# Optimization experiments

Measured on AMD Instinct MI355X. Metric: run time of the kernel, lower is better.

Reference implementation:

```python
import jax, jax.numpy as jnp
import numpy as np

N_NODES = 50000


def _relgraphconv(x, W, Wloop, b, src, dst, etypes, n_nodes):
    # DGL RelGraphConv (regularizer=None, self_loop=True, norm=None):
    # out[i] = sum over incoming edges (j->i, rel r) of W_r @ x[j]  +  W_loop @ x[i]  +  b
    # low-mem form: transform all nodes per relation, then gather per edge.
    h_rel = jnp.einsum('ni,rio->rno', x, W)          # [R, N, out]
    msg = h_rel[etypes, src]                          # [E, out]
    agg = jax.ops.segment_sum(msg, dst, num_segments=n_nodes)  # [N, out]
    return agg + x @ Wloop + b


def setup_inputs() -> dict:
    key = jax.random.key(0)
    ks = jax.random.split(key, 12)
    N, E, n_state = N_NODES, 800000, 128
    inp = {
        'x': jax.random.normal(ks[0], (N, n_state), dtype=jnp.float32),
        'src': jax.random.randint(ks[1], (E,), 0, N, dtype=jnp.int32),
        'dst': jax.random.randint(ks[2], (E,), 0, N, dtype=jnp.int32),
        'etypes': jax.random.randint(ks[3], (E,), 0, 2, dtype=jnp.int32),
        'cell_size': jax.random.randint(ks[4], (N,), 0, 8, dtype=jnp.int32),
        'max_size': jax.random.randint(ks[5], (N,), 0, 8, dtype=jnp.int32),
        'W1': jax.random.normal(ks[6], (2, n_state, 64), dtype=jnp.float32) * 0.05,
        'loop1': jax.random.normal(ks[7], (n_state, 64), dtype=jnp.float32) * 0.05,
        'b1': jnp.zeros((64,), dtype=jnp.float32),
        'W2': jax.random.normal(ks[8], (2, 64, 64), dtype=jnp.float32) * 0.05,
        'loop2': jax.random.normal(ks[9], (64, 64), dtype=jnp.float32) * 0.05,
        'b2': jnp.zeros((64,), dtype=jnp.float32),
        'W3': jax.random.normal(ks[10], (2, 64, 2), dtype=jnp.float32) * 0.05,
        'loop3': jax.random.normal(ks[11], (64, 2), dtype=jnp.float32) * 0.05,
        'b3': jnp.zeros((2,), dtype=jnp.float32),
    }
    return inp


def reference(x, src, dst, etypes, cell_size, max_size,
              W1, loop1, b1, W2, loop2, b2, W3, loop3, b3):
    N = x.shape[0]
    h = jax.nn.relu(_relgraphconv(x, W1, loop1, b1, src, dst, etypes, N))
    h = jax.nn.relu(_relgraphconv(h, W2, loop2, b2, src, dst, etypes, N))
    h = _relgraphconv(h, W3, loop3, b3, src, dst, etypes, N)   # [N, 2]
    # action mask: col 0 = cannot upsize, col 1 = cannot downsize
    upper = cell_size >= (max_size - 1)
    lower = cell_size == 0
    mask = jnp.stack([upper, lower], axis=1)                   # [N, 2] bool
    return jnp.where(mask, h.min() - 1.0, h)
```

## Files before the change

### kernel.cpp

```cpp
#include <hip/hip_runtime.h>


#define STRIDE 64

typedef unsigned short ushortT;

__device__ inline ushortT f2bf(float f) {
    union { float f; unsigned u; } v; v.f = f;
    unsigned r = v.u + 0x7FFFu + ((v.u >> 16) & 1u);
    return (ushortT)(r >> 16);
}
__device__ inline float bf2f(ushortT h) {
    union { unsigned u; float f; } v; v.u = ((unsigned)h) << 16;
    return v.f;
}

__device__ inline void atomicMinF(float* addr, float v) {
    if (v >= 0.f) atomicMin((int*)addr, __float_as_int(v));
    else          atomicMax((unsigned int*)addr, __float_as_uint(v));
}

__global__ __launch_bounds__(256) void mega1_kernel(
    const float* __restrict__ x, const float* __restrict__ W1,
    const float* __restrict__ loop1, const float* __restrict__ b1,
    ushortT* __restrict__ hrelb, ushortT* __restrict__ H1b,
    const int* __restrict__ src, const int* __restrict__ dst,
    const int* __restrict__ et, int* __restrict__ cnt, int* __restrict__ eidx,
    int N, int E) {
    if (blockIdx.x & 1) {
        int g = (int)(blockIdx.x >> 1);
        int e0 = g * 1024 + (int)threadIdx.x;
        int e1 = e0 + 256, e2 = e0 + 512, e3 = e0 + 768;
        bool a0 = e0 < E, a1 = e1 < E, a2 = e2 < E, a3 = e3 < E;
        int d0 = a0 ? dst[e0] : 0, d1 = a1 ? dst[e1] : 0;
        int d2 = a2 ? dst[e2] : 0, d3 = a3 ? dst[e3] : 0;
        int v0 = a0 ? (et[e0] * N + src[e0]) : 0;
        int v1 = a1 ? (et[e1] * N + src[e1]) : 0;
        int v2 = a2 ? (et[e2] * N + src[e2]) : 0;
        int v3 = a3 ? (et[e3] * N + src[e3]) : 0;
        int p0 = 0, p1 = 0, p2 = 0, p3 = 0;
        if (a0) p0 = atomicAdd(&cnt[d0], 1);
        if (a1) p1 = atomicAdd(&cnt[d1], 1);
        if (a2) p2 = atomicAdd(&cnt[d2], 1);
        if (a3) p3 = atomicAdd(&cnt[d3], 1);
        if (a0 && p0 < STRIDE) eidx[(size_t)d0 * STRIDE + p0] = v0;
        if (a1 && p1 < STRIDE) eidx[(size_t)d1 * STRIDE + p1] = v1;
        if (a2 && p2 < STRIDE) eidx[(size_t)d2 * STRIDE + p2] = v2;
        if (a3 && p3 < STRIDE) eidx[(size_t)d3 * STRIDE + p3] = v3;
        return;
    }
    __shared__ float xs[64][64];
    __shared__ ushortT wsb[3][64][68];
    const int tile = (int)(blockIdx.x >> 1);
    const int nbase = tile * 64;
    const int t = (int)threadIdx.x;
    const int tx = t & 15, ty = t >> 4;

    float acc[3][4][4];
#pragma unroll
    for (int m = 0; m < 3; ++m)
#pragma unroll
        for (int j = 0; j < 4; ++j)
#pragma unroll
            for (int i = 0; i < 4; ++i) acc[m][j][i] = 0.f;

    for (int kt = 0; kt < 2; ++kt) {
#pragma unroll
        for (int j = 0; j < 4; ++j) {
            int i = t + j * 256;
            int node = i >> 4;
            int kk4 = (i & 15) * 4;
            int n = nbase + node;
            float4 g = make_float4(0.f, 0.f, 0.f, 0.f);
            if (n < N) g = *(const float4*)&x[(size_t)n * 128 + kt * 64 + kk4];
            int pc = (node + kk4) & 63;
            xs[kk4 + 0][pc] = g.x;
            xs[kk4 + 1][pc] = g.y;
            xs[kk4 + 2][pc] = g.z;
            xs[kk4 + 3][pc] = g.w;
        }
#pragma unroll
        for (int j = 0; j < 12; ++j) {
            int i = t + j * 256;
            int mat = i >> 10;
            int rc = i & 1023;
            int kk = rc >> 4;
            int c4 = (rc & 15) * 4;
            const float* Wm = (mat < 2) ? (W1 + ((size_t)mat * 128 + kt * 64 + kk) * 64 + c4)
                                        : (loop1 + ((size_t)kt * 64 + kk) * 64 + c4);
            float4 g = *(const float4*)Wm;
            ushort4 o;
            o.x = f2bf(g.x); o.y = f2bf(g.y); o.z = f2bf(g.z); o.w = f2bf(g.w);
            *(ushort4*)&wsb[mat][kk][c4] = o;
        }
        __syncthreads();

#pragma unroll 4
        for (int kk = 0; kk < 64; ++kk) {
            int kb = kk & ~3;
            float4 a = *(const float4*)&xs[kk][(ty * 4 + kb) & 63];
#pragma unroll
            for (int m = 0; m < 3; ++m) {
                ushort4 wu = *(const ushort4*)&wsb[m][kk][tx * 4];
                float w0 = bf2f(wu.x), w1 = bf2f(wu.y), w2 = bf2f(wu.z), w3 = bf2f(wu.w);
                acc[m][0][0] += a.x * w0; acc[m][0][1] += a.x * w1; acc[m][0][2] += a.x * w2; acc[m][0][3] += a.x * w3;
                acc[m][1][0] += a.y * w0; acc[m][1][1] += a.y * w1; acc[m][1][2] += a.y * w2; acc[m][1][3] += a.y * w3;
                acc[m][2][0] += a.z * w0; acc[m][2][1] += a.z * w1; acc[m][2][2] += a.z * w2; acc[m][2][3] += a.z * w3;
                acc[m][3][0] += a.w * w0; acc[m][3][1] += a.w * w1; acc[m][3][2] += a.w * w2; acc[m][3][3] += a.w * w3;
            }
        }
        __syncthreads();
    }

    float b0 = b1[tx * 4 + 0], bb1 = b1[tx * 4 + 1], b2v = b1[tx * 4 + 2], b3v = b1[tx * 4 + 3];
#pragma unroll
    for (int j = 0; j < 4; ++j) {
        int n = nbase + ty * 4 + j;
        if (n < N) {
#pragma unroll
            for (int m = 0; m < 2; ++m) {
                ushort4 o;
                o.x = f2bf(acc[m][j][0]); o.y = f2bf(acc[m][j][1]);
                o.z = f2bf(acc[m][j][2]); o.w = f2bf(acc[m][j][3]);
                *(ushort4*)&hrelb[((size_t)m * N + n) * 64 + tx * 4] = o;
            }
            ushort4 h;
            h.x = f2bf(acc[2][j][0] + b0);  h.y = f2bf(acc[2][j][1] + bb1);
            h.z = f2bf(acc[2][j][2] + b2v); h.w = f2bf(acc[2][j][3] + b3v);
            *(ushort4*)&H1b[(size_t)n * 64 + tx * 4] = h;
        }
    }
}

__global__ void agg1_kernel(const ushortT* __restrict__ hrelb, const int* __restrict__ eidx,
                            const int* __restrict__ cnt, ushortT* __restrict__ H1b, int N) {
    int node = (int)blockIdx.x * 4 + ((int)threadIdx.x >> 6);
    if (node >= N) return;
    int lane = (int)threadIdx.x & 63;
    int deg = min(cnt[node], STRIDE);
    int my = (lane < deg) ? eidx[(size_t)node * STRIDE + lane] : 0;
    float acc = bf2f(H1b[(size_t)node * 64 + lane]);
    int j = 0;
    for (; j + 3 < deg; j += 4) {
        int i0 = __shfl(my, j, 64), i1 = __shfl(my, j + 1, 64);
        int i2 = __shfl(my, j + 2, 64), i3 = __shfl(my, j + 3, 64);
        float v0 = bf2f(hrelb[(size_t)i0 * 64 + lane]);
        float v1 = bf2f(hrelb[(size_t)i1 * 64 + lane]);
        float v2 = bf2f(hrelb[(size_t)i2 * 64 + lane]);
        float v3 = bf2f(hrelb[(size_t)i3 * 64 + lane]);
        acc += (v0 + v1) + (v2 + v3);
    }
    for (; j < deg; ++j)
        acc += bf2f(hrelb[(size_t)__shfl(my, j, 64) * 64 + lane]);
    H1b[(size_t)node * 64 + lane] = f2bf(fmaxf(acc, 0.f));
}

__global__ __launch_bounds__(256) void gemm2_kernel(
    const ushortT* __restrict__ H1b,
    const float* __restrict__ W2, const float* __restrict__ loop2,
    const float* __restrict__ b2,
    ushortT* __restrict__ hrel2b, float* __restrict__ H2, int N) {
    __shared__ float xs[64][65];
    __shared__ ushortT wsb[3][64][68];
    const int t = (int)threadIdx.x;
    const int nbase = (int)blockIdx.x * 64;

#pragma unroll
    for (int j = 0; j < 12; ++j) {
        int i = t + j * 256;
        int mat = i >> 10;
        int rc = i & 1023;
        int kk = rc >> 4;
        int c4 = (rc & 15) * 4;
        const float* Wm = (mat < 2) ? (W2 + ((size_t)mat * 64 + kk) * 64 + c4)
                                    : (loop2 + (size_t)kk * 64 + c4);
        float4 g = *(const float4*)Wm;
        ushort4 o;
        o.x = f2bf(g.x); o.y = f2bf(g.y); o.z = f2bf(g.z); o.w = f2bf(g.w);
        *(ushort4*)&wsb[mat][kk][c4] = o;
    }
#pragma unroll
    for (int j = 0; j < 4; ++j) {
        int i = t + j * 256;
        int node = i >> 4;
        int k4 = (i & 15) * 4;
        int n = nbase + node;
        ushort4 g = make_ushort4(0, 0, 0, 0);
        if (n < N) g = *(const ushort4*)&H1b[(size_t)n * 64 + k4];
        xs[node][k4 + 0] = bf2f(g.x);
        xs[node][k4 + 1] = bf2f(g.y);
        xs[node][k4 + 2] = bf2f(g.z);
        xs[node][k4 + 3] = bf2f(g.w);
    }
    __syncthreads();

    const int tx = t & 15, ty = t >> 4;
    float acc2[3][4][4];
#pragma unroll
    for (int m = 0; m < 3; ++m)
#pragma unroll
        for (int j = 0; j < 4; ++j)
#pragma unroll
            for (int i = 0; i < 4; ++i) acc2[m][j][i] = 0.f;

#pragma unroll 4
    for (int kk = 0; kk < 64; ++kk) {
        float a0 = xs[ty * 4 + 0][kk];
        float a1 = xs[ty * 4 + 1][kk];
        float a2 = xs[ty * 4 + 2][kk];
        float a3 = xs[ty * 4 + 3][kk];
#pragma unroll
        for (int m = 0; m < 3; ++m) {
            ushort4 wu = *(const ushort4*)&wsb[m][kk][tx * 4];
            float w0 = bf2f(wu.x), w1 = bf2f(wu.y), w2 = bf2f(wu.z), w3 = bf2f(wu.w);
            acc2[m][0][0] += a0 * w0; acc2[m][0][1] += a0 * w1; acc2[m][0][2] += a0 * w2; acc2[m][0][3] += a0 * w3;
            acc2[m][1][0] += a1 * w0; acc2[m][1][1] += a1 * w1; acc2[m][1][2] += a1 * w2; acc2[m][1][3] += a1 * w3;
            acc2[m][2][0] += a2 * w0; acc2[m][2][1] += a2 * w1; acc2[m][2][2] += a2 * w2; acc2[m][2][3] += a2 * w3;
            acc2[m][3][0] += a3 * w0; acc2[m][3][1] += a3 * w1; acc2[m][3][2] += a3 * w2; acc2[m][3][3] += a3 * w3;
        }
    }

    float b0 = b2[tx * 4 + 0], bb1 = b2[tx * 4 + 1], b2v = b2[tx * 4 + 2], b3v = b2[tx * 4 + 3];
#pragma unroll
    for (int j = 0; j < 4; ++j) {
        int n = nbase + ty * 4 + j;
        if (n < N) {
#pragma unroll
            for (int m = 0; m < 2; ++m) {
                ushort4 o;
                o.x = f2bf(acc2[m][j][0]); o.y = f2bf(acc2[m][j][1]);
                o.z = f2bf(acc2[m][j][2]); o.w = f2bf(acc2[m][j][3]);
                *(ushort4*)&hrel2b[((size_t)m * N + n) * 64 + tx * 4] = o;
            }
            float4 h = make_float4(acc2[2][j][0] + b0, acc2[2][j][1] + bb1,
                                   acc2[2][j][2] + b2v, acc2[2][j][3] + b3v);
            *(float4*)&H2[(size_t)n * 64 + tx * 4] = h;
        }
    }
}

__global__ void k3_kernel(const ushortT* __restrict__ hrel2b, const float* __restrict__ H2,
                          const int* __restrict__ eidx, const int* __restrict__ cnt,
                          const float* __restrict__ W3, const float* __restrict__ loop3,
                          const float* __restrict__ b3,
                          float* __restrict__ hrel3, float* __restrict__ H3, int N) {
    int node = (int)blockIdx.x * 4 + ((int)threadIdx.x >> 6);
    if (node >= N) return;
    int lane = (int)threadIdx.x & 63;
    int deg = min(cnt[node], STRIDE);
    int my = (lane < deg) ? eidx[(size_t)node * STRIDE + lane] : 0;
    float acc = H2[(size_t)node * 64 + lane];
    int j = 0;
    for (; j + 3 < deg; j += 4) {
        int i0 = __shfl(my, j, 64), i1 = __shfl(my, j + 1, 64);
        int i2 = __shfl(my, j + 2, 64), i3 = __shfl(my, j + 3, 64);
        float v0 = bf2f(hrel2b[(size_t)i0 * 64 + lane]);
        float v1 = bf2f(hrel2b[(size_t)i1 * 64 + lane]);
        float v2 = bf2f(hrel2b[(size_t)i2 * 64 + lane]);
        float v3 = bf2f(hrel2b[(size_t)i3 * 64 + lane]);
        acc += (v0 + v1) + (v2 + v3);
    }
    for (; j < deg; ++j)
        acc += bf2f(hrel2b[(size_t)__shfl(my, j, 64) * 64 + lane]);
    float xk = fmaxf(acc, 0.f);
    float p[6];
    p[0] = xk * W3[lane * 2 + 0];
    p[1] = xk * W3[lane * 2 + 1];
    p[2] = xk * W3[(64 + lane) * 2 + 0];
    p[3] = xk * W3[(64 + lane) * 2 + 1];
    p[4] = xk * loop3[lane * 2 + 0];
    p[5] = xk * loop3[lane * 2 + 1];
#pragma unroll
    for (int m = 32; m >= 1; m >>= 1) {
#pragma unroll
        for (int q = 0; q < 6; ++q) p[q] += __shfl_xor(p[q], m, 64);
    }
    if (lane == 0) {
        hrel3[(size_t)node * 2 + 0] = p[0];
        hrel3[(size_t)node * 2 + 1] = p[1];
        hrel3[((size_t)N + node) * 2 + 0] = p[2];
        hrel3[((size_t)N + node) * 2 + 1] = p[3];
        H3[(size_t)node * 2 + 0] = p[4] + b3[0];
        H3[(size_t)node * 2 + 1] = p[5] + b3[1];
    }
}

__global__ void agg3min_kernel(const float* __restrict__ hrel3, const int* __restrict__ eidx,
                               const int* __restrict__ cnt, float* __restrict__ H3,
                               float* __restrict__ minval, int N) {
    int n = (int)blockIdx.x * 256 + (int)threadIdx.x;
    float v = 3.4e38f;
    if (n < N) {
        float a0 = H3[n * 2 + 0], a1 = H3[n * 2 + 1];
        int deg = min(cnt[n], STRIDE);
        const int* row = &eidx[(size_t)n * STRIDE];
        int j = 0;
        for (; j + 3 < deg; j += 4) {
            int i0 = row[j], i1 = row[j + 1], i2 = row[j + 2], i3 = row[j + 3];
            float2 q0 = *(const float2*)&hrel3[(size_t)i0 * 2];
            float2 q1 = *(const float2*)&hrel3[(size_t)i1 * 2];
            float2 q2 = *(const float2*)&hrel3[(size_t)i2 * 2];
            float2 q3 = *(const float2*)&hrel3[(size_t)i3 * 2];
            a0 += (q0.x + q1.x) + (q2.x + q3.x);
            a1 += (q0.y + q1.y) + (q2.y + q3.y);
        }
        for (; j < deg; ++j) {
            float2 q = *(const float2*)&hrel3[(size_t)row[j] * 2];
            a0 += q.x; a1 += q.y;
        }
        H3[n * 2 + 0] = a0;
        H3[n * 2 + 1] = a1;
        v = fminf(a0, a1);
    }
#pragma unroll
    for (int m = 32; m >= 1; m >>= 1) v = fminf(v, __shfl_xor(v, m, 64));
    __shared__ float s[4];
    if ((threadIdx.x & 63) == 0) s[threadIdx.x >> 6] = v;
    __syncthreads();
    if (threadIdx.x == 0)
        atomicMinF(minval, fminf(fminf(s[0], s[1]), fminf(s[2], s[3])));
}

__global__ void mask_kernel(const float* __restrict__ H3, const float* __restrict__ minval,
                            const int* __restrict__ cs, const int* __restrict__ ms,
                            float* __restrict__ out, int N) {
    int n = (int)blockIdx.x * 256 + (int)threadIdx.x;
    if (n >= N) return;
    float m = minval[0] - 1.0f;
    bool up = cs[n] >= ms[n] - 1;
    bool lo = cs[n] == 0;
    out[n * 2 + 0] = up ? m : H3[n * 2 + 0];
    out[n * 2 + 1] = lo ? m : H3[n * 2 + 1];
}

extern "C" void kernel_launch(void* const* d_in, const int* in_sizes, int n_in,
                              void* d_out, int out_size, void* d_ws, size_t ws_size,
                              hipStream_t stream) {
    const float* x     = (const float*)d_in[0];
    const int* src     = (const int*)d_in[1];
    const int* dst     = (const int*)d_in[2];
    const int* etypes  = (const int*)d_in[3];
    const int* cellsz  = (const int*)d_in[4];
    const int* maxsz   = (const int*)d_in[5];
    const float* W1    = (const float*)d_in[6];
    const float* loop1 = (const float*)d_in[7];
    const float* b1    = (const float*)d_in[8];
    const float* W2    = (const float*)d_in[9];
    const float* loop2 = (const float*)d_in[10];
    const float* b2    = (const float*)d_in[11];
    const float* W3    = (const float*)d_in[12];
    const float* loop3 = (const float*)d_in[13];
    const float* b3    = (const float*)d_in[14];
    float* out = (float*)d_out;

    const int N = in_sizes[0] / 128;
    const int E = in_sizes[1];

    char* p = (char*)d_ws;
    auto alloc = [&](size_t bytes) -> void* {
        void* r = (void*)p;
        p += ((bytes + 255) / 256) * 256;
        return r;
    };
    ushortT* hrelb  = (ushortT*)alloc((size_t)2 * N * 64 * 2);
    ushortT* H1b    = (ushortT*)alloc((size_t)N * 64 * 2);
    ushortT* hrel2b = (ushortT*)alloc((size_t)2 * N * 64 * 2);
    float* H2       = (float*)alloc((size_t)N * 64 * 4);
    float* hrel3    = (float*)alloc((size_t)2 * N * 2 * 4);
    float* H3       = (float*)alloc((size_t)N * 2 * 4);
    int* cnt        = (int*)alloc((size_t)N * 4);
    int* eidx       = (int*)alloc((size_t)N * STRIDE * 4);
    float* minval   = (float*)alloc(4);
    (void)ws_size; (void)n_in; (void)out_size;

    const int NB_N   = (N + 255) / 256;
    const int NTILES = (N + 63) / 64;
    const int NB_W   = (N + 3) / 4;

    hipMemsetAsync(cnt, 0, (size_t)N * 4, stream);
    hipMemsetAsync(minval, 0x7f, 4, stream);

    mega1_kernel<<<NTILES * 2, 256, 0, stream>>>(
        x, W1, loop1, b1, hrelb, H1b, src, dst, etypes, cnt, eidx, N, E);

    agg1_kernel<<<NB_W, 256, 0, stream>>>(hrelb, eidx, cnt, H1b, N);

    gemm2_kernel<<<NTILES, 256, 0, stream>>>(H1b, W2, loop2, b2, hrel2b, H2, N);

    k3_kernel<<<NB_W, 256, 0, stream>>>(hrel2b, H2, eidx, cnt, W3, loop3, b3,
                                        hrel3, H3, N);

    agg3min_kernel<<<NB_N, 256, 0, stream>>>(hrel3, eidx, cnt, H3, minval, N);
    mask_kernel<<<NB_N, 256, 0, stream>>>(H3, minval, cellsz, maxsz, out, N);
}
```

Baseline: 268.8 us.

## Split fused scatter/GEMM kernel, store activations in LDS as bf16, unroll gathers by eight

The combined kernel, which interleaved edge-scatter blocks with layer-1 GEMM tiles, is split into two separate kernels, adding one launch. Both GEMM kernels now hold the activation tile in shared memory as bf16 instead of fp32, halving LDS footprint and store traffic. The cost is extra conversions in the inner loop and a precision loss on x in layer 1. The two gather-aggregation kernels unroll the neighbor loop from four to eight to keep more loads in flight.

```diff
diff --git a/kernel.cpp b/kernel.cpp
--- a/kernel.cpp
+++ b/kernel.cpp
@@ -20,39 +20,37 @@
     else          atomicMax((unsigned int*)addr, __float_as_uint(v));
 }
 
-__global__ __launch_bounds__(256) void mega1_kernel(
-    const float* __restrict__ x, const float* __restrict__ W1,
-    const float* __restrict__ loop1, const float* __restrict__ b1,
-    ushortT* __restrict__ hrelb, ushortT* __restrict__ H1b,
+__global__ __launch_bounds__(256) void scatter_kernel(
     const int* __restrict__ src, const int* __restrict__ dst,
     const int* __restrict__ et, int* __restrict__ cnt, int* __restrict__ eidx,
     int N, int E) {
-    if (blockIdx.x & 1) {
-        int g = (int)(blockIdx.x >> 1);
-        int e0 = g * 1024 + (int)threadIdx.x;
-        int e1 = e0 + 256, e2 = e0 + 512, e3 = e0 + 768;
-        bool a0 = e0 < E, a1 = e1 < E, a2 = e2 < E, a3 = e3 < E;
-        int d0 = a0 ? dst[e0] : 0, d1 = a1 ? dst[e1] : 0;
-        int d2 = a2 ? dst[e2] : 0, d3 = a3 ? dst[e3] : 0;
-        int v0 = a0 ? (et[e0] * N + src[e0]) : 0;
-        int v1 = a1 ? (et[e1] * N + src[e1]) : 0;
-        int v2 = a2 ? (et[e2] * N + src[e2]) : 0;
-        int v3 = a3 ? (et[e3] * N + src[e3]) : 0;
-        int p0 = 0, p1 = 0, p2 = 0, p3 = 0;
-        if (a0) p0 = atomicAdd(&cnt[d0], 1);
-        if (a1) p1 = atomicAdd(&cnt[d1], 1);
-        if (a2) p2 = atomicAdd(&cnt[d2], 1);
-        if (a3) p3 = atomicAdd(&cnt[d3], 1);
-        if (a0 && p0 < STRIDE) eidx[(size_t)d0 * STRIDE + p0] = v0;
-        if (a1 && p1 < STRIDE) eidx[(size_t)d1 * STRIDE + p1] = v1;
-        if (a2 && p2 < STRIDE) eidx[(size_t)d2 * STRIDE + p2] = v2;
-        if (a3 && p3 < STRIDE) eidx[(size_t)d3 * STRIDE + p3] = v3;
-        return;
-    }
-    __shared__ float xs[64][64];
+    int e0 = (int)blockIdx.x * 1024 + (int)threadIdx.x;
+    int e1 = e0 + 256, e2 = e0 + 512, e3 = e0 + 768;
+    bool a0 = e0 < E, a1 = e1 < E, a2 = e2 < E, a3 = e3 < E;
+    int d0 = a0 ? dst[e0] : 0, d1 = a1 ? dst[e1] : 0;
+    int d2 = a2 ? dst[e2] : 0, d3 = a3 ? dst[e3] : 0;
+    int v0 = a0 ? (et[e0] * N + src[e0]) : 0;
+    int v1 = a1 ? (et[e1] * N + src[e1]) : 0;
+    int v2 = a2 ? (et[e2] * N + src[e2]) : 0;
+    int v3 = a3 ? (et[e3] * N + src[e3]) : 0;
+    int p0 = 0, p1 = 0, p2 = 0, p3 = 0;
+    if (a0) p0 = atomicAdd(&cnt[d0], 1);
+    if (a1) p1 = atomicAdd(&cnt[d1], 1);
+    if (a2) p2 = atomicAdd(&cnt[d2], 1);
+    if (a3) p3 = atomicAdd(&cnt[d3], 1);
+    if (a0 && p0 < STRIDE) eidx[(size_t)d0 * STRIDE + p0] = v0;
+    if (a1 && p1 < STRIDE) eidx[(size_t)d1 * STRIDE + p1] = v1;
+    if (a2 && p2 < STRIDE) eidx[(size_t)d2 * STRIDE + p2] = v2;
+    if (a3 && p3 < STRIDE) eidx[(size_t)d3 * STRIDE + p3] = v3;
+}
+
+__global__ __launch_bounds__(256) void gemm1_kernel(
+    const float* __restrict__ x, const float* __restrict__ W1,
+    const float* __restrict__ loop1, const float* __restrict__ b1,
+    ushortT* __restrict__ hrelb, ushortT* __restrict__ H1b, int N) {
+    __shared__ ushortT xsb[64][64];
     __shared__ ushortT wsb[3][64][68];
-    const int tile = (int)(blockIdx.x >> 1);
-    const int nbase = tile * 64;
+    const int nbase = (int)blockIdx.x * 64;
     const int t = (int)threadIdx.x;
     const int tx = t & 15, ty = t >> 4;
 
@@ -74,10 +72,10 @@
             float4 g = make_float4(0.f, 0.f, 0.f, 0.f);
             if (n < N) g = *(const float4*)&x[(size_t)n * 128 + kt * 64 + kk4];
             int pc = (node + kk4) & 63;
-            xs[kk4 + 0][pc] = g.x;
-            xs[kk4 + 1][pc] = g.y;
-            xs[kk4 + 2][pc] = g.z;
-            xs[kk4 + 3][pc] = g.w;
+            xsb[kk4 + 0][pc] = f2bf(g.x);
+            xsb[kk4 + 1][pc] = f2bf(g.y);
+            xsb[kk4 + 2][pc] = f2bf(g.z);
+            xsb[kk4 + 3][pc] = f2bf(g.w);
         }
 #pragma unroll
         for (int j = 0; j < 12; ++j) {
@@ -98,15 +96,16 @@
 #pragma unroll 4
         for (int kk = 0; kk < 64; ++kk) {
             int kb = kk & ~3;
-            float4 a = *(const float4*)&xs[kk][(ty * 4 + kb) & 63];
+            ushort4 au = *(const ushort4*)&xsb[kk][(ty * 4 + kb) & 63];
+            float ax = bf2f(au.x), ay = bf2f(au.y), az = bf2f(au.z), aw = bf2f(au.w);
 #pragma unroll
             for (int m = 0; m < 3; ++m) {
                 ushort4 wu = *(const ushort4*)&wsb[m][kk][tx * 4];
                 float w0 = bf2f(wu.x), w1 = bf2f(wu.y), w2 = bf2f(wu.z), w3 = bf2f(wu.w);
-                acc[m][0][0] += a.x * w0; acc[m][0][1] += a.x * w1; acc[m][0][2] += a.x * w2; acc[m][0][3] += a.x * w3;
-                acc[m][1][0] += a.y * w0; acc[m][1][1] += a.y * w1; acc[m][1][2] += a.y * w2; acc[m][1][3] += a.y * w3;
-                acc[m][2][0] += a.z * w0; acc[m][2][1] += a.z * w1; acc[m][2][2] += a.z * w2; acc[m][2][3] += a.z * w3;
-                acc[m][3][0] += a.w * w0; acc[m][3][1] += a.w * w1; acc[m][3][2] += a.w * w2; acc[m][3][3] += a.w * w3;
+                acc[m][0][0] += ax * w0; acc[m][0][1] += ax * w1; acc[m][0][2] += ax * w2; acc[m][0][3] += ax * w3;
+                acc[m][1][0] += ay * w0; acc[m][1][1] += ay * w1; acc[m][1][2] += ay * w2; acc[m][1][3] += ay * w3;
+                acc[m][2][0] += az * w0; acc[m][2][1] += az * w1; acc[m][2][2] += az * w2; acc[m][2][3] += az * w3;
+                acc[m][3][0] += aw * w0; acc[m][3][1] += aw * w1; acc[m][3][2] += aw * w2; acc[m][3][3] += aw * w3;
             }
         }
         __syncthreads();
@@ -141,14 +140,14 @@
     int my = (lane < deg) ? eidx[(size_t)node * STRIDE + lane] : 0;
     float acc = bf2f(H1b[(size_t)node * 64 + lane]);
     int j = 0;
-    for (; j + 3 < deg; j += 4) {
-        int i0 = __shfl(my, j, 64), i1 = __shfl(my, j + 1, 64);
-        int i2 = __shfl(my, j + 2, 64), i3 = __shfl(my, j + 3, 64);
-        float v0 = bf2f(hrelb[(size_t)i0 * 64 + lane]);
-        float v1 = bf2f(hrelb[(size_t)i1 * 64 + lane]);
-        float v2 = bf2f(hrelb[(size_t)i2 * 64 + lane]);
-        float v3 = bf2f(hrelb[(size_t)i3 * 64 + lane]);
-        acc += (v0 + v1) + (v2 + v3);
+    for (; j + 7 < deg; j += 8) {
+        int id[8];
+        float v[8];
+#pragma unroll
+        for (int q = 0; q < 8; ++q) id[q] = __shfl(my, j + q, 64);
+#pragma unroll
+        for (int q = 0; q < 8; ++q) v[q] = bf2f(hrelb[(size_t)id[q] * 64 + lane]);
+        acc += ((v[0] + v[1]) + (v[2] + v[3])) + ((v[4] + v[5]) + (v[6] + v[7]));
     }
     for (; j < deg; ++j)
         acc += bf2f(hrelb[(size_t)__shfl(my, j, 64) * 64 + lane]);
@@ -160,7 +159,7 @@
     const float* __restrict__ W2, const float* __restrict__ loop2,
     const float* __restrict__ b2,
     ushortT* __restrict__ hrel2b, float* __restrict__ H2, int N) {
-    __shared__ float xs[64][65];
+    __shared__ ushortT xsb[64][66];
     __shared__ ushortT wsb[3][64][68];
     const int t = (int)threadIdx.x;
     const int nbase = (int)blockIdx.x * 64;
@@ -187,10 +186,7 @@
         int n = nbase + node;
         ushort4 g = make_ushort4(0, 0, 0, 0);
         if (n < N) g = *(const ushort4*)&H1b[(size_t)n * 64 + k4];
-        xs[node][k4 + 0] = bf2f(g.x);
-        xs[node][k4 + 1] = bf2f(g.y);
-        xs[node][k4 + 2] = bf2f(g.z);
-        xs[node][k4 + 3] = bf2f(g.w);
+        *(ushort4*)&xsb[node][k4] = g;
     }
     __syncthreads();
 
@@ -205,10 +201,10 @@
 
 #pragma unroll 4
     for (int kk = 0; kk < 64; ++kk) {
-        float a0 = xs[ty * 4 + 0][kk];
-        float a1 = xs[ty * 4 + 1][kk];
-        float a2 = xs[ty * 4 + 2][kk];
-        float a3 = xs[ty * 4 + 3][kk];
+        float a0 = bf2f(xsb[ty * 4 + 0][kk]);
+        float a1 = bf2f(xsb[ty * 4 + 1][kk]);
+        float a2 = bf2f(xsb[ty * 4 + 2][kk]);
+        float a3 = bf2f(xsb[ty * 4 + 3][kk]);
 #pragma unroll
         for (int m = 0; m < 3; ++m) {
             ushort4 wu = *(const ushort4*)&wsb[m][kk][tx * 4];
@@ -251,14 +247,14 @@
     int my = (lane < deg) ? eidx[(size_t)node * STRIDE + lane] : 0;
     float acc = H2[(size_t)node * 64 + lane];
     int j = 0;
-    for (; j + 3 < deg; j += 4) {
-        int i0 = __shfl(my, j, 64), i1 = __shfl(my, j + 1, 64);
-        int i2 = __shfl(my, j + 2, 64), i3 = __shfl(my, j + 3, 64);
-        float v0 = bf2f(hrel2b[(size_t)i0 * 64 + lane]);
-        float v1 = bf2f(hrel2b[(size_t)i1 * 64 + lane]);
-        float v2 = bf2f(hrel2b[(size_t)i2 * 64 + lane]);
-        float v3 = bf2f(hrel2b[(size_t)i3 * 64 + lane]);
-        acc += (v0 + v1) + (v2 + v3);
+    for (; j + 7 < deg; j += 8) {
+        int id[8];
+        float v[8];
+#pragma unroll
+        for (int q = 0; q < 8; ++q) id[q] = __shfl(my, j + q, 64);
+#pragma unroll
+        for (int q = 0; q < 8; ++q) v[q] = bf2f(hrel2b[(size_t)id[q] * 64 + lane]);
+        acc += ((v[0] + v[1]) + (v[2] + v[3])) + ((v[4] + v[5]) + (v[6] + v[7]));
     }
     for (; j < deg; ++j)
         acc += bf2f(hrel2b[(size_t)__shfl(my, j, 64) * 64 + lane]);
@@ -376,12 +372,14 @@
     const int NB_N   = (N + 255) / 256;
     const int NTILES = (N + 63) / 64;
     const int NB_W   = (N + 3) / 4;
+    const int NB_SC  = (E + 1023) / 1024;
 
     hipMemsetAsync(cnt, 0, (size_t)N * 4, stream);
     hipMemsetAsync(minval, 0x7f, 4, stream);
 
-    mega1_kernel<<<NTILES * 2, 256, 0, stream>>>(
-        x, W1, loop1, b1, hrelb, H1b, src, dst, etypes, cnt, eidx, N, E);
+    scatter_kernel<<<NB_SC, 256, 0, stream>>>(src, dst, etypes, cnt, eidx, N, E);
+
+    gemm1_kernel<<<NTILES, 256, 0, stream>>>(x, W1, loop1, b1, hrelb, H1b, N);
 
     agg1_kernel<<<NB_W, 256, 0, stream>>>(hrelb, eidx, cnt, H1b, N);
 
```

After: 295.4 us. 9.9% more time.
